# Kernel tuning notes

Hardware: AMD Instinct MI355X
Metric: run time of the kernel (lower is better)

Reference implementation:

```python
import jax, jax.numpy as jnp
import numpy as np

B, N = 8, 2048
DIN, DH, DE = 32, 64, 64
R = 3          # number_relations
L = 3          # num_layers -> 1 first + 1 block + 1 last
PRED_IN = DH * (L - 1) + DE  # concat: 64*2 + 64 = 192
EPS_BN = 1e-5
EPS_NORM = 1e-12


def setup_inputs() -> dict:
    key = jax.random.key(0)
    ks = jax.random.split(key, 12)
    x = jax.random.normal(ks[0], (B, N, DIN), jnp.float32)
    # relation labels in {0..R}; 0 = no edge, 1..R = relation type
    relation = jax.random.randint(ks[1], (B, N, N), 0, R + 1).astype(jnp.int32)
    # adjacency is the 0/1 edge indicator (float), as the torch code treats it
    adj = (relation > 0).astype(jnp.float32)
    s = 0.05
    w_first = jax.random.normal(ks[2], (R, DIN, DH), jnp.float32) * s
    b_first = jnp.zeros((DH,), jnp.float32)
    w_block = jax.random.normal(ks[3], (R, DH, DH), jnp.float32) * s
    b_block = jnp.zeros((DH,), jnp.float32)
    w_last = jax.random.normal(ks[4], (R, DH, DE), jnp.float32) * s
    b_last = jnp.zeros((DE,), jnp.float32)
    w_map = jax.random.normal(ks[5], (PRED_IN, DE), jnp.float32) * s
    b_map = jnp.zeros((DE,), jnp.float32)
    return {"x": x, "relation": relation, "adj": adj,
            "w_first": w_first, "b_first": b_first,
            "w_block": w_block, "b_block": b_block,
            "w_last": w_last, "b_last": b_last,
            "w_map": w_map, "b_map": b_map}


def _graph_conv(x, rel, W, b):
    # rel: [B,N,N] (int labels or float adjacency); W: [R, din, dout]
    y = jnp.zeros((x.shape[0], x.shape[1], W.shape[2]), x.dtype)
    for i in range(R):  # fixed, small relation count
        mask = (rel == (i + 1)).astype(x.dtype)            # [B,N,N]
        h = jnp.einsum('bij,bjd->bid', mask, x)            # masked aggregation
        y = y + jnp.einsum('bid,de->bie', h, W[i])
    y = y + b
    # F.normalize(p=2, dim=2): v / max(||v||, eps)
    nrm = jnp.sqrt(jnp.sum(y * y, axis=2, keepdims=True))
    return y / jnp.maximum(nrm, EPS_NORM)


def _apply_bn(x):
    # fresh BatchNorm1d(N) in training mode, affine weight=1/bias=0:
    # normalize over (batch, feature) per node index, biased variance
    mean = jnp.mean(x, axis=(0, 2), keepdims=True)
    var = jnp.mean(jnp.square(x - mean), axis=(0, 2), keepdims=True)
    return (x - mean) * jax.lax.rsqrt(var + EPS_BN)


def reference(x, relation, adj, w_first, b_first, w_block, b_block,
              w_last, b_last, w_map, b_map):
    # conv_first uses `relation`
    h = _apply_bn(jax.nn.relu(_graph_conv(x, relation, w_first, b_first)))
    out_all = [jnp.max(h, axis=1)]
    # conv_block and conv_last are (faithfully) called with `adj` as relation
    h = _apply_bn(jax.nn.relu(_graph_conv(h, adj, w_block, b_block)))
    out_all.append(jnp.max(h, axis=1))
    h = _graph_conv(h, adj, w_last, b_last)
    out_all.append(jnp.max(h, axis=1))
    output = jnp.concatenate(out_all, axis=1)        # [B, PRED_IN]
    ypred = output @ w_map + b_map                   # map_model Linear
    return (output, ypred)
```

## Files before the change

### kernel.cpp

```cpp
#include <hip/hip_runtime.h>


#define NN 2048
#define PLANE_W 1048576L

typedef short short8 __attribute__((ext_vector_type(8)));
typedef float floatx4 __attribute__((ext_vector_type(4)));

__device__ __forceinline__ unsigned short f2bf(float x) {
  unsigned u = __float_as_uint(x);
  u += 0x7FFFu + ((u >> 16) & 1u);
  return (unsigned short)(u >> 16);
}

__device__ void dev_xw_first(char* smemc, int u, int tid,
                             const float* __restrict__ x,
                             const float* __restrict__ w,
                             unsigned short* __restrict__ xws) {
  float* xs = (float*)smemc;
  float* wsh = (float*)(smemc + 64 * 33 * 4);
  const int jc = u & 31, b = (u >> 5) & 7, r = u >> 8;
  const int j0 = jc * 64;
  for (int idx = tid; idx < 64 * 32; idx += 256) {
    int row = idx >> 5, f = idx & 31;
    xs[row * 33 + f] = x[((long)b * NN + j0 + row) * 32 + f];
    wsh[idx] = w[r * 2048 + idx];
  }
  __syncthreads();
  const int j = tid & 63, g = tid >> 6;
  const int k = j0 + j;
  const int kblk = k >> 5, kq = (k >> 3) & 3, kj = k & 7;
  unsigned short* dst =
      xws + (((long)(r * 8 + b) * 64 + kblk) * 4 + g) * 512 + kj;
  float xr[32];
#pragma unroll
  for (int f = 0; f < 32; ++f) xr[f] = xs[j * 33 + f];
#pragma unroll
  for (int ii = 0; ii < 16; ++ii) {
    float acc = 0.f;
#pragma unroll
    for (int f = 0; f < 32; ++f) acc += xr[f] * wsh[f * 64 + g * 16 + ii];
    dst[(kq * 16 + ii) * 8] = f2bf(acc);
  }
  __syncthreads();
}

__global__ __launch_bounds__(256) void k_pack_xw1(const int* __restrict__ rel,
                                                  unsigned* __restrict__ planes,
                                                  const float* __restrict__ x,
                                                  const float* __restrict__ w,
                                                  unsigned short* __restrict__ xws) {
  __shared__ __align__(16) char smem[16640];
  const int bid = blockIdx.x, tid = threadIdx.x;
  if (bid < 768) dev_xw_first(smem, bid, tid, x, w, xws);
  for (long t = (long)bid * 256 + tid; t < 1048576L; t += 4096L * 256) {
    int w32 = (int)(t & 63);
    long bi = t >> 6;
    const int4* rp = (const int4*)(rel + bi * NN + w32 * 32);
    unsigned m0 = 0, m1 = 0, m2 = 0;
#pragma unroll
    for (int c = 0; c < 8; ++c) {
      int4 v = rp[c];
      int vv[4] = {v.x, v.y, v.z, v.w};
#pragma unroll
      for (int j = 0; j < 4; ++j) {
        unsigned b1 = 1u << (c * 4 + j);
        m0 |= (vv[j] == 1) ? b1 : 0u;
        m1 |= (vv[j] == 2) ? b1 : 0u;
        m2 |= (vv[j] == 3) ? b1 : 0u;
      }
    }
    long o = bi * 64 + w32;
    planes[o] = m0;
    planes[PLANE_W + o] = m1;
    planes[2 * PLANE_W + o] = m2;
  }
}

template <int NREL, bool RELU, bool POOL3>
__global__ __launch_bounds__(256) void k_gemm_f(
    const unsigned* __restrict__ planes, const unsigned short* __restrict__ xws,
    const float* __restrict__ bias, float* __restrict__ Hout,
    float* __restrict__ part3) {
  constexpr int SMEM = (NREL * 16640 > 32768) ? NREL * 16640 : 32768;
  __shared__ __align__(16) char smem[SMEM];
  unsigned* mw = (unsigned*)smem;
  floatx4* cb = (floatx4*)smem;
  const int bid = blockIdx.x;
  const int b = bid & 7, it = bid >> 3;
  const int tid = threadIdx.x;
  const int wave = tid >> 6, lane = tid & 63;
  const int m = lane & 15, kq = lane >> 4;
  const int i0 = it * 64;

  for (int idx = tid; idx < NREL * 4096; idx += 256) {
    int p = idx >> 12, rem = idx & 4095, row = rem >> 6, w = rem & 63;
    long g = ((long)b * NN + i0 + row) * 64 + w;
    unsigned v;
    if (NREL == 3)
      v = planes[(long)p * PLANE_W + g];
    else
      v = planes[g] | planes[PLANE_W + g] | planes[2 * PLANE_W + g];
    mw[(p * 64 + row) * 65 + w] = v;
  }
  __syncthreads();

  floatx4 acc[4][4];
#pragma unroll
  for (int rs = 0; rs < 4; ++rs)
#pragma unroll
    for (int t = 0; t < 4; ++t) acc[rs][t] = floatx4{0, 0, 0, 0};

  short8 bf[2][NREL][4];
  {
    const int kblk0 = wave * 16;
#pragma unroll
    for (int p = 0; p < NREL; ++p) {
      const unsigned short* bb =
          xws + ((long)(p * 8 + b) * 64 + kblk0) * 2048 + lane * 8;
#pragma unroll
      for (int t = 0; t < 4; ++t) bf[0][p][t] = *(const short8*)(bb + t * 512);
    }
  }
#pragma unroll 2
  for (int qq = 0; qq < 16; ++qq) {
    const int cur = qq & 1, nxt = cur ^ 1;
    if (qq < 15) {
      const int kblkn = wave * 16 + qq + 1;
#pragma unroll
      for (int p = 0; p < NREL; ++p) {
        const unsigned short* bb =
            xws + ((long)(p * 8 + b) * 64 + kblkn) * 2048 + lane * 8;
#pragma unroll
        for (int t = 0; t < 4; ++t)
          bf[nxt][p][t] = *(const short8*)(bb + t * 512);
      }
    }
    const int kblk = wave * 16 + qq;
#pragma unroll
    for (int p = 0; p < NREL; ++p) {
#pragma unroll
      for (int rs = 0; rs < 4; ++rs) {
        unsigned word = mw[(p * 64 + rs * 16 + m) * 65 + kblk];
        unsigned byte = (word >> (kq * 8)) & 0xffu;
        unsigned pp = byte | (byte << 15);
        union {
          unsigned uu[4];
          short8 s8;
        } fr;
        unsigned w0 = pp & 0x00010001u;
        fr.uu[0] = (w0 << 14) - (w0 << 7);
        unsigned w1 = pp & 0x00040004u;
        fr.uu[1] = (w1 << 12) - (w1 << 5);
        unsigned w2 = pp & 0x00100010u;
        fr.uu[2] = (w2 << 10) - (w2 << 3);
        unsigned w3 = pp & 0x00400040u;
        fr.uu[3] = (w3 << 8) - (w3 << 1);
#pragma unroll
        for (int t = 0; t < 4; ++t)
          acc[rs][t] = __builtin_amdgcn_mfma_f32_16x16x32_bf16(
              fr.s8, bf[cur][p][t], acc[rs][t], 0, 0, 0);
      }
    }
  }
  __syncthreads();

  if (wave >= 2) {
    floatx4* dst = cb + (wave - 2) * 1024;
#pragma unroll
    for (int rs = 0; rs < 4; ++rs)
#pragma unroll
      for (int t = 0; t < 4; ++t) dst[(rs * 4 + t) * 64 + lane] = acc[rs][t];
  }
  __syncthreads();
  if (wave < 2) {
    floatx4* src = cb + wave * 1024;
#pragma unroll
    for (int rs = 0; rs < 4; ++rs)
#pragma unroll
      for (int t = 0; t < 4; ++t) acc[rs][t] += src[(rs * 4 + t) * 64 + lane];
  }
  __syncthreads();
  if (wave == 1) {
#pragma unroll
    for (int rs = 0; rs < 4; ++rs)
#pragma unroll
      for (int t = 0; t < 4; ++t) cb[(rs * 4 + t) * 64 + lane] = acc[rs][t];
  }
  __syncthreads();
  if (wave == 0) {
#pragma unroll
    for (int rs = 0; rs < 4; ++rs)
#pragma unroll
      for (int t = 0; t < 4; ++t) acc[rs][t] += cb[(rs * 4 + t) * 64 + lane];
    float bv[4];
#pragma unroll
    for (int t = 0; t < 4; ++t) bv[t] = bias[t * 16 + m];
    float pmt[4] = {-3.4e38f, -3.4e38f, -3.4e38f, -3.4e38f};
#pragma unroll
    for (int rs = 0; rs < 4; ++rs) {
      float ss[4];
#pragma unroll
      for (int reg = 0; reg < 4; ++reg) {
#pragma unroll
        for (int t = 0; t < 4; ++t) acc[rs][t][reg] += bv[t];
        ss[reg] = acc[rs][0][reg] * acc[rs][0][reg] +
                  acc[rs][1][reg] * acc[rs][1][reg] +
                  acc[rs][2][reg] * acc[rs][2][reg] +
                  acc[rs][3][reg] * acc[rs][3][reg];
#pragma unroll
        for (int off = 1; off <= 8; off <<= 1)
          ss[reg] += __shfl_xor(ss[reg], off);
        ss[reg] = 1.0f / fmaxf(sqrtf(ss[reg]), 1e-12f);
      }
#pragma unroll
      for (int t = 0; t < 4; ++t) {
#pragma unroll
        for (int reg = 0; reg < 4; ++reg) {
          float o = acc[rs][t][reg] * ss[reg];
          if (RELU) o = fmaxf(o, 0.0f);
          if (POOL3)
            pmt[t] = fmaxf(pmt[t], o);
          else
            Hout[((long)b * NN + i0 + rs * 16 + kq * 4 + reg) * 64 + t * 16 + m] = o;
        }
      }
    }
    if (POOL3) {
#pragma unroll
      for (int t = 0; t < 4; ++t) {
        pmt[t] = fmaxf(pmt[t], __shfl_xor(pmt[t], 16));
        pmt[t] = fmaxf(pmt[t], __shfl_xor(pmt[t], 32));
      }
      if (kq == 0) {
#pragma unroll
        for (int t = 0; t < 4; ++t)
          part3[((long)b * 32 + it) * 64 + t * 16 + m] = pmt[t];
      }
    }
  }
}

__global__ __launch_bounds__(256) void k_bn(const float* __restrict__ Hs,
                                            float* __restrict__ HBNs,
                                            float* __restrict__ PP) {
  __shared__ float red[8];
  __shared__ float nv0[512];
  const int bid = blockIdx.x, tid = threadIdx.x;
  const int lane = tid & 63, wv = tid >> 6;
  const int wl = (wv & 1) * 64 + lane;
  const int flat0 = wl * 4;
  const int b = flat0 >> 6, e0 = flat0 & 63;
  const int np = bid;
  const int node = np * 2 + (wv >> 1);
  const float4 hv = *(const float4*)(Hs + ((long)b * NN + node) * 64 + e0);
  float s1 = hv.x + hv.y + hv.z + hv.w;
  float s2 = hv.x * hv.x + hv.y * hv.y + hv.z * hv.z + hv.w * hv.w;
#pragma unroll
  for (int off = 32; off >= 1; off >>= 1) {
    s1 += __shfl_xor(s1, off);
    s2 += __shfl_xor(s2, off);
  }
  if (lane == 0) {
    red[wv * 2] = s1;
    red[wv * 2 + 1] = s2;
  }
  __syncthreads();
  const int pb = (wv >> 1) * 4;
  float S1 = red[pb] + red[pb + 2];
  float S2 = red[pb + 1] + red[pb + 3];
  float mean = S1 * (1.0f / 512.0f);
  float var = fmaxf(S2 * (1.0f / 512.0f) - mean * mean, 0.0f);
  float rs = rsqrtf(var + 1e-5f);
  float4 nv;
  nv.x = (hv.x - mean) * rs;
  nv.y = (hv.y - mean) * rs;
  nv.z = (hv.z - mean) * rs;
  nv.w = (hv.w - mean) * rs;
  *(float4*)(HBNs + ((long)b * NN + node) * 64 + e0) = nv;
  if (wv < 2) *(float4*)(nv0 + flat0) = nv;
  __syncthreads();
  if (wv >= 2) {
    float4 ov = *(const float4*)(nv0 + flat0);
    float4 mx;
    mx.x = fmaxf(nv.x, ov.x);
    mx.y = fmaxf(nv.y, ov.y);
    mx.z = fmaxf(nv.z, ov.z);
    mx.w = fmaxf(nv.w, ov.w);
    *(float4*)(PP + (long)np * 512 + flat0) = mx;
  }
}

__global__ __launch_bounds__(256) void k_xwh_pf(const float* __restrict__ hsrc,
                                                const float* __restrict__ w,
                                                unsigned short* __restrict__ xws,
                                                const float* __restrict__ PP,
                                                float* __restrict__ out, int ofs) {
  __shared__ __align__(16) char smemc[33024];
  const int bid = blockIdx.x, tid = threadIdx.x;
  if (bid < 256) {
    float* hs = (float*)smemc;
    float* wsh = (float*)(smemc + 16640);
    const int jc = bid & 31, b = bid >> 5;
    const int j0 = jc * 64;
    for (int idx = tid; idx < 4096; idx += 256) {
      int row = idx >> 6, f = idx & 63;
      hs[row * 65 + f] = hsrc[((long)b * NN + j0 + row) * 64 + f];
      wsh[idx] = w[idx];
    }
    __syncthreads();
    const int j = tid & 63, g = tid >> 6;
    const int k = j0 + j;
    const int kblk = k >> 5, kq = (k >> 3) & 3, kj = k & 7;
    unsigned short* dst = xws + (((long)b * 64 + kblk) * 4 + g) * 512 + kj;
    float acc[16];
#pragma unroll
    for (int ii = 0; ii < 16; ++ii) acc[ii] = 0.f;
#pragma unroll
    for (int c = 0; c < 4; ++c) {
      float xr[16];
#pragma unroll
      for (int f = 0; f < 16; ++f) xr[f] = hs[j * 65 + c * 16 + f];
#pragma unroll
      for (int ii = 0; ii < 16; ++ii)
#pragma unroll
        for (int f = 0; f < 16; ++f)
          acc[ii] += xr[f] * wsh[(c * 16 + f) * 64 + g * 16 + ii];
    }
#pragma unroll
    for (int ii = 0; ii < 16; ++ii) dst[(kq * 16 + ii) * 8] = f2bf(acc[ii]);
  } else {
    const int b = bid - 256;
    const int e = tid & 63, q = tid >> 6;
    float m = -3.4e38f;
    for (int blk = q; blk < 1024; blk += 4)
      m = fmaxf(m, PP[(long)blk * 512 + b * 64 + e]);
    float* pmx = (float*)smemc;
    pmx[q * 64 + e] = m;
    __syncthreads();
    if (q == 0)
      out[b * 192 + ofs + e] =
          fmaxf(fmaxf(pmx[e], pmx[64 + e]), fmaxf(pmx[128 + e], pmx[192 + e]));
  }
}

__global__ __launch_bounds__(512) void k_tail(const float* __restrict__ P3,
                                              float* __restrict__ out,
                                              const float* __restrict__ wmap,
                                              const float* __restrict__ bmap) {
  const int b = threadIdx.x >> 6, e = threadIdx.x & 63;
  float m = -3.4e38f;
#pragma unroll
  for (int c = 0; c < 32; ++c) m = fmaxf(m, P3[((long)b * 32 + c) * 64 + e]);
  out[b * 192 + 128 + e] = m;
  __syncthreads();
  float acc = bmap[e];
  for (int k = 0; k < 192; ++k) acc += out[b * 192 + k] * wmap[k * 64 + e];
  out[1536 + b * 64 + e] = acc;
}

extern "C" void kernel_launch(void* const* d_in, const int* in_sizes, int n_in,
                              void* d_out, int out_size, void* d_ws,
                              size_t ws_size, hipStream_t stream) {
  const float* x = (const float*)d_in[0];
  const int* rel = (const int*)d_in[1];
  const float* w_first = (const float*)d_in[3];
  const float* b_first = (const float*)d_in[4];
  const float* w_block = (const float*)d_in[5];
  const float* b_block = (const float*)d_in[6];
  const float* w_last = (const float*)d_in[7];
  const float* b_last = (const float*)d_in[8];
  const float* w_map = (const float*)d_in[9];
  const float* b_map = (const float*)d_in[10];
  float* out = (float*)d_out;

  char* ws = (char*)d_ws;
  const size_t MB = 1024 * 1024;
  unsigned* PLANES = (unsigned*)(ws);
  unsigned short* XWS = (unsigned short*)(ws + 12 * MB);
  float* H = (float*)(ws + 18 * MB);
  float* HBN = (float*)(ws + 22 * MB);
  float* PARTP = (float*)(ws + 26 * MB);
  float* PART3 = (float*)(ws + 28 * MB);

  k_pack_xw1<<<4096, 256, 0, stream>>>(rel, PLANES, x, w_first, XWS);
  k_gemm_f<3, true, false><<<256, 256, 0, stream>>>(PLANES, XWS, b_first, H,
                                                    nullptr);
  k_bn<<<1024, 256, 0, stream>>>(H, HBN, PARTP);
  k_xwh_pf<<<264, 256, 0, stream>>>(HBN, w_block, XWS, PARTP, out, 0);
  k_gemm_f<1, true, false><<<256, 256, 0, stream>>>(PLANES, XWS, b_block, H,
                                                    nullptr);
  k_bn<<<1024, 256, 0, stream>>>(H, HBN, PARTP);
  k_xwh_pf<<<264, 256, 0, stream>>>(HBN, w_last, XWS, PARTP, out, 64);
  k_gemm_f<1, false, true><<<256, 256, 0, stream>>>(PLANES, XWS, b_last,
                                                    nullptr, PART3);
  k_tail<<<1, 512, 0, stream>>>(PART3, out, w_map, b_map);
}
```

Measured before the change: 427.8 us.

## Fuse batchnorm into XW transform and widen aggregation GEMM to eight waves

The separate batchnorm kernel is folded into the XW-transform kernel: each block recomputes the per-node mean and variance over all batches, normalizes in shared memory, and writes per-node-chunk max partials. The pooled max reductions for layers one and two move into the tail kernel. The masked-aggregation GEMM now runs 512 threads (8 waves) with the bitmask tile loaded in two K chunks and a serial cross-wave reduction. This removes two launches and the HBN round trip through memory, at the cost of redundant statistics reads across batch blocks and more synchronisation in the reduction.

```diff
diff --git a/kernel.cpp b/kernel.cpp
--- a/kernel.cpp
+++ b/kernel.cpp
@@ -78,11 +78,11 @@
 }
 
 template <int NREL, bool RELU, bool POOL3>
-__global__ __launch_bounds__(256) void k_gemm_f(
+__global__ __launch_bounds__(512) void k_gemm8(
     const unsigned* __restrict__ planes, const unsigned short* __restrict__ xws,
     const float* __restrict__ bias, float* __restrict__ Hout,
     float* __restrict__ part3) {
-  constexpr int SMEM = (NREL * 16640 > 32768) ? NREL * 16640 : 32768;
+  constexpr int SMEM = (NREL * 8448 > 16640) ? NREL * 8448 : 16640;
   __shared__ __align__(16) char smem[SMEM];
   unsigned* mw = (unsigned*)smem;
   floatx4* cb = (floatx4*)smem;
@@ -93,101 +93,86 @@
   const int m = lane & 15, kq = lane >> 4;
   const int i0 = it * 64;
 
-  for (int idx = tid; idx < NREL * 4096; idx += 256) {
-    int p = idx >> 12, rem = idx & 4095, row = rem >> 6, w = rem & 63;
-    long g = ((long)b * NN + i0 + row) * 64 + w;
-    unsigned v;
-    if (NREL == 3)
-      v = planes[(long)p * PLANE_W + g];
-    else
-      v = planes[g] | planes[PLANE_W + g] | planes[2 * PLANE_W + g];
-    mw[(p * 64 + row) * 65 + w] = v;
-  }
-  __syncthreads();
-
   floatx4 acc[4][4];
 #pragma unroll
   for (int rs = 0; rs < 4; ++rs)
 #pragma unroll
     for (int t = 0; t < 4; ++t) acc[rs][t] = floatx4{0, 0, 0, 0};
 
-  short8 bf[2][NREL][4];
-  {
-    const int kblk0 = wave * 16;
-#pragma unroll
-    for (int p = 0; p < NREL; ++p) {
-      const unsigned short* bb =
-          xws + ((long)(p * 8 + b) * 64 + kblk0) * 2048 + lane * 8;
-#pragma unroll
-      for (int t = 0; t < 4; ++t) bf[0][p][t] = *(const short8*)(bb + t * 512);
-    }
-  }
-#pragma unroll 2
-  for (int qq = 0; qq < 16; ++qq) {
-    const int cur = qq & 1, nxt = cur ^ 1;
-    if (qq < 15) {
-      const int kblkn = wave * 16 + qq + 1;
+  for (int chunk = 0; chunk < 2; ++chunk) {
+    for (int idx = tid; idx < NREL * 2048; idx += 512) {
+      int p = idx >> 11, rem = idx & 2047, row = rem >> 5, w = rem & 31;
+      long g = ((long)b * NN + i0 + row) * 64 + chunk * 32 + w;
+      unsigned v;
+      if (NREL == 3)
+        v = planes[(long)p * PLANE_W + g];
+      else
+        v = planes[g] | planes[PLANE_W + g] | planes[2 * PLANE_W + g];
+      mw[(p * 64 + row) * 33 + w] = v;
+    }
+    __syncthreads();
+#pragma unroll
+    for (int j = 0; j < 4; ++j) {
+      const int kk = j * 8 + wave;
+      const int kblk = chunk * 32 + kk;
 #pragma unroll
       for (int p = 0; p < NREL; ++p) {
         const unsigned short* bb =
-            xws + ((long)(p * 8 + b) * 64 + kblkn) * 2048 + lane * 8;
-#pragma unroll
-        for (int t = 0; t < 4; ++t)
-          bf[nxt][p][t] = *(const short8*)(bb + t * 512);
-      }
-    }
-    const int kblk = wave * 16 + qq;
-#pragma unroll
-    for (int p = 0; p < NREL; ++p) {
-#pragma unroll
-      for (int rs = 0; rs < 4; ++rs) {
-        unsigned word = mw[(p * 64 + rs * 16 + m) * 65 + kblk];
-        unsigned byte = (word >> (kq * 8)) & 0xffu;
-        unsigned pp = byte | (byte << 15);
-        union {
-          unsigned uu[4];
-          short8 s8;
-        } fr;
-        unsigned w0 = pp & 0x00010001u;
-        fr.uu[0] = (w0 << 14) - (w0 << 7);
-        unsigned w1 = pp & 0x00040004u;
-        fr.uu[1] = (w1 << 12) - (w1 << 5);
-        unsigned w2 = pp & 0x00100010u;
-        fr.uu[2] = (w2 << 10) - (w2 << 3);
-        unsigned w3 = pp & 0x00400040u;
-        fr.uu[3] = (w3 << 8) - (w3 << 1);
-#pragma unroll
-        for (int t = 0; t < 4; ++t)
-          acc[rs][t] = __builtin_amdgcn_mfma_f32_16x16x32_bf16(
-              fr.s8, bf[cur][p][t], acc[rs][t], 0, 0, 0);
-      }
-    }
-  }
-  __syncthreads();
-
-  if (wave >= 2) {
-    floatx4* dst = cb + (wave - 2) * 1024;
-#pragma unroll
-    for (int rs = 0; rs < 4; ++rs)
-#pragma unroll
-      for (int t = 0; t < 4; ++t) dst[(rs * 4 + t) * 64 + lane] = acc[rs][t];
-  }
-  __syncthreads();
-  if (wave < 2) {
-    floatx4* src = cb + wave * 1024;
-#pragma unroll
-    for (int rs = 0; rs < 4; ++rs)
-#pragma unroll
-      for (int t = 0; t < 4; ++t) acc[rs][t] += src[(rs * 4 + t) * 64 + lane];
-  }
-  __syncthreads();
-  if (wave == 1) {
-#pragma unroll
-    for (int rs = 0; rs < 4; ++rs)
-#pragma unroll
-      for (int t = 0; t < 4; ++t) cb[(rs * 4 + t) * 64 + lane] = acc[rs][t];
-  }
-  __syncthreads();
+            xws + ((long)(p * 8 + b) * 64 + kblk) * 2048 + lane * 8;
+        short8 bf0 = *(const short8*)(bb);
+        short8 bf1 = *(const short8*)(bb + 512);
+        short8 bf2 = *(const short8*)(bb + 1024);
+        short8 bf3 = *(const short8*)(bb + 1536);
+#pragma unroll
+        for (int rs = 0; rs < 4; ++rs) {
+          unsigned word = mw[(p * 64 + rs * 16 + m) * 33 + kk];
+          unsigned byte = (word >> (kq * 8)) & 0xffu;
+          unsigned pp = byte | (byte << 15);
+          union {
+            unsigned uu[4];
+            short8 s8;
+          } fr;
+          unsigned w0 = pp & 0x00010001u;
+          fr.uu[0] = (w0 << 14) - (w0 << 7);
+          unsigned w1 = pp & 0x00040004u;
+          fr.uu[1] = (w1 << 12) - (w1 << 5);
+          unsigned w2 = pp & 0x00100010u;
+          fr.uu[2] = (w2 << 10) - (w2 << 3);
+          unsigned w3 = pp & 0x00400040u;
+          fr.uu[3] = (w3 << 8) - (w3 << 1);
+          acc[rs][0] = __builtin_amdgcn_mfma_f32_16x16x32_bf16(fr.s8, bf0,
+                                                              acc[rs][0], 0, 0, 0);
+          acc[rs][1] = __builtin_amdgcn_mfma_f32_16x16x32_bf16(fr.s8, bf1,
+                                                              acc[rs][1], 0, 0, 0);
+          acc[rs][2] = __builtin_amdgcn_mfma_f32_16x16x32_bf16(fr.s8, bf2,
+                                                              acc[rs][2], 0, 0, 0);
+          acc[rs][3] = __builtin_amdgcn_mfma_f32_16x16x32_bf16(fr.s8, bf3,
+                                                              acc[rs][3], 0, 0, 0);
+        }
+      }
+    }
+    __syncthreads();
+  }
+
+  for (int k = 7; k >= 1; --k) {
+    if (wave == k) {
+      if (k == 7) {
+#pragma unroll
+        for (int rs = 0; rs < 4; ++rs)
+#pragma unroll
+          for (int t = 0; t < 4; ++t) cb[(rs * 4 + t) * 64 + lane] = acc[rs][t];
+      } else {
+#pragma unroll
+        for (int rs = 0; rs < 4; ++rs)
+#pragma unroll
+          for (int t = 0; t < 4; ++t) {
+            floatx4 v = cb[(rs * 4 + t) * 64 + lane];
+            cb[(rs * 4 + t) * 64 + lane] = v + acc[rs][t];
+          }
+      }
+    }
+    __syncthreads();
+  }
   if (wave == 0) {
 #pragma unroll
     for (int rs = 0; rs < 4; ++rs)
@@ -241,74 +226,50 @@
   }
 }
 
-__global__ __launch_bounds__(256) void k_bn(const float* __restrict__ Hs,
-                                            float* __restrict__ HBNs,
-                                            float* __restrict__ PP) {
-  __shared__ float red[8];
-  __shared__ float nv0[512];
-  const int bid = blockIdx.x, tid = threadIdx.x;
-  const int lane = tid & 63, wv = tid >> 6;
-  const int wl = (wv & 1) * 64 + lane;
-  const int flat0 = wl * 4;
-  const int b = flat0 >> 6, e0 = flat0 & 63;
-  const int np = bid;
-  const int node = np * 2 + (wv >> 1);
-  const float4 hv = *(const float4*)(Hs + ((long)b * NN + node) * 64 + e0);
-  float s1 = hv.x + hv.y + hv.z + hv.w;
-  float s2 = hv.x * hv.x + hv.y * hv.y + hv.z * hv.z + hv.w * hv.w;
-#pragma unroll
-  for (int off = 32; off >= 1; off >>= 1) {
-    s1 += __shfl_xor(s1, off);
-    s2 += __shfl_xor(s2, off);
-  }
-  if (lane == 0) {
-    red[wv * 2] = s1;
-    red[wv * 2 + 1] = s2;
-  }
-  __syncthreads();
-  const int pb = (wv >> 1) * 4;
-  float S1 = red[pb] + red[pb + 2];
-  float S2 = red[pb + 1] + red[pb + 3];
-  float mean = S1 * (1.0f / 512.0f);
-  float var = fmaxf(S2 * (1.0f / 512.0f) - mean * mean, 0.0f);
-  float rs = rsqrtf(var + 1e-5f);
-  float4 nv;
-  nv.x = (hv.x - mean) * rs;
-  nv.y = (hv.y - mean) * rs;
-  nv.z = (hv.z - mean) * rs;
-  nv.w = (hv.w - mean) * rs;
-  *(float4*)(HBNs + ((long)b * NN + node) * 64 + e0) = nv;
-  if (wv < 2) *(float4*)(nv0 + flat0) = nv;
-  __syncthreads();
-  if (wv >= 2) {
-    float4 ov = *(const float4*)(nv0 + flat0);
-    float4 mx;
-    mx.x = fmaxf(nv.x, ov.x);
-    mx.y = fmaxf(nv.y, ov.y);
-    mx.z = fmaxf(nv.z, ov.z);
-    mx.w = fmaxf(nv.w, ov.w);
-    *(float4*)(PP + (long)np * 512 + flat0) = mx;
-  }
-}
-
-__global__ __launch_bounds__(256) void k_xwh_pf(const float* __restrict__ hsrc,
+__global__ __launch_bounds__(256) void k_xwh_bn(const float* __restrict__ H,
                                                 const float* __restrict__ w,
                                                 unsigned short* __restrict__ xws,
-                                                const float* __restrict__ PP,
-                                                float* __restrict__ out, int ofs) {
-  __shared__ __align__(16) char smemc[33024];
+                                                float* __restrict__ PP) {
+  __shared__ float hs[64 * 65];
+  __shared__ float wsh[64 * 64];
+  __shared__ float sm[64], srs[64];
   const int bid = blockIdx.x, tid = threadIdx.x;
-  if (bid < 256) {
-    float* hs = (float*)smemc;
-    float* wsh = (float*)(smemc + 16640);
-    const int jc = bid & 31, b = bid >> 5;
-    const int j0 = jc * 64;
-    for (int idx = tid; idx < 4096; idx += 256) {
-      int row = idx >> 6, f = idx & 63;
-      hs[row * 65 + f] = hsrc[((long)b * NN + j0 + row) * 64 + f];
-      wsh[idx] = w[idx];
-    }
-    __syncthreads();
+  const int jc = bid & 31, b = bid >> 5;
+  const int j0 = jc * 64;
+  {
+    const int n = tid >> 2, q = tid & 3;
+    float s1 = 0.f, s2 = 0.f;
+#pragma unroll
+    for (int bb = 0; bb < 8; ++bb) {
+      const float4* hp =
+          (const float4*)(H + ((long)bb * NN + j0 + n) * 64 + q * 16);
+#pragma unroll
+      for (int c = 0; c < 4; ++c) {
+        float4 v = hp[c];
+        s1 += v.x + v.y + v.z + v.w;
+        s2 += v.x * v.x + v.y * v.y + v.z * v.z + v.w * v.w;
+      }
+    }
+    s1 += __shfl_xor(s1, 1);
+    s2 += __shfl_xor(s2, 1);
+    s1 += __shfl_xor(s1, 2);
+    s2 += __shfl_xor(s2, 2);
+    if (q == 0) {
+      float mean = s1 * (1.0f / 512.0f);
+      float var = fmaxf(s2 * (1.0f / 512.0f) - mean * mean, 0.0f);
+      sm[n] = mean;
+      srs[n] = rsqrtf(var + 1e-5f);
+    }
+  }
+  __syncthreads();
+  for (int idx = tid; idx < 4096; idx += 256) {
+    int row = idx >> 6, f = idx & 63;
+    float v = H[((long)b * NN + j0 + row) * 64 + f];
+    hs[row * 65 + f] = (v - sm[row]) * srs[row];
+    wsh[idx] = w[idx];
+  }
+  __syncthreads();
+  {
     const int j = tid & 63, g = tid >> 6;
     const int k = j0 + j;
     const int kblk = k >> 5, kq = (k >> 3) & 3, kj = k & 7;
@@ -329,34 +290,44 @@
     }
 #pragma unroll
     for (int ii = 0; ii < 16; ++ii) dst[(kq * 16 + ii) * 8] = f2bf(acc[ii]);
-  } else {
-    const int b = bid - 256;
-    const int e = tid & 63, q = tid >> 6;
-    float m = -3.4e38f;
-    for (int blk = q; blk < 1024; blk += 4)
-      m = fmaxf(m, PP[(long)blk * 512 + b * 64 + e]);
-    float* pmx = (float*)smemc;
-    pmx[q * 64 + e] = m;
-    __syncthreads();
-    if (q == 0)
-      out[b * 192 + ofs + e] =
-          fmaxf(fmaxf(pmx[e], pmx[64 + e]), fmaxf(pmx[128 + e], pmx[192 + e]));
-  }
-}
-
-__global__ __launch_bounds__(512) void k_tail(const float* __restrict__ P3,
+  }
+  if (b == 0) {
+#pragma unroll
+    for (int part = 0; part < 2; ++part) {
+      const int col = part * 256 + tid;
+      const int bb = col >> 6, e = col & 63;
+      float mx = -3.4e38f;
+      for (int n = 0; n < 64; ++n) {
+        float v = H[((long)bb * NN + j0 + n) * 64 + e];
+        mx = fmaxf(mx, (v - sm[n]) * srs[n]);
+      }
+      PP[(long)jc * 512 + col] = mx;
+    }
+  }
+}
+
+__global__ __launch_bounds__(512) void k_tail(const float* __restrict__ PP1,
+                                              const float* __restrict__ PP2,
+                                              const float* __restrict__ P3,
                                               float* __restrict__ out,
                                               const float* __restrict__ wmap,
                                               const float* __restrict__ bmap) {
-  const int b = threadIdx.x >> 6, e = threadIdx.x & 63;
-  float m = -3.4e38f;
-#pragma unroll
-  for (int c = 0; c < 32; ++c) m = fmaxf(m, P3[((long)b * 32 + c) * 64 + e]);
-  out[b * 192 + 128 + e] = m;
+  const int col = threadIdx.x;
+  const int bb = col >> 6, e = col & 63;
+  float m1 = -3.4e38f, m2 = -3.4e38f, m3 = -3.4e38f;
+#pragma unroll
+  for (int c = 0; c < 32; ++c) {
+    m1 = fmaxf(m1, PP1[(long)c * 512 + col]);
+    m2 = fmaxf(m2, PP2[(long)c * 512 + col]);
+    m3 = fmaxf(m3, P3[((long)bb * 32 + c) * 64 + e]);
+  }
+  out[bb * 192 + e] = m1;
+  out[bb * 192 + 64 + e] = m2;
+  out[bb * 192 + 128 + e] = m3;
   __syncthreads();
   float acc = bmap[e];
-  for (int k = 0; k < 192; ++k) acc += out[b * 192 + k] * wmap[k * 64 + e];
-  out[1536 + b * 64 + e] = acc;
+  for (int k = 0; k < 192; ++k) acc += out[bb * 192 + k] * wmap[k * 64 + e];
+  out[1536 + bb * 64 + e] = acc;
 }
 
 extern "C" void kernel_launch(void* const* d_in, const int* in_sizes, int n_in,
@@ -379,20 +350,18 @@
   unsigned* PLANES = (unsigned*)(ws);
   unsigned short* XWS = (unsigned short*)(ws + 12 * MB);
   float* H = (float*)(ws + 18 * MB);
-  float* HBN = (float*)(ws + 22 * MB);
-  float* PARTP = (float*)(ws + 26 * MB);
-  float* PART3 = (float*)(ws + 28 * MB);
+  float* PP1 = (float*)(ws + 22 * MB);
+  float* PP2 = (float*)(ws + 23 * MB);
+  float* PART3 = (float*)(ws + 24 * MB);
 
   k_pack_xw1<<<4096, 256, 0, stream>>>(rel, PLANES, x, w_first, XWS);
-  k_gemm_f<3, true, false><<<256, 256, 0, stream>>>(PLANES, XWS, b_first, H,
-                                                    nullptr);
-  k_bn<<<1024, 256, 0, stream>>>(H, HBN, PARTP);
-  k_xwh_pf<<<264, 256, 0, stream>>>(HBN, w_block, XWS, PARTP, out, 0);
-  k_gemm_f<1, true, false><<<256, 256, 0, stream>>>(PLANES, XWS, b_block, H,
-                                                    nullptr);
-  k_bn<<<1024, 256, 0, stream>>>(H, HBN, PARTP);
-  k_xwh_pf<<<264, 256, 0, stream>>>(HBN, w_last, XWS, PARTP, out, 64);
-  k_gemm_f<1, false, true><<<256, 256, 0, stream>>>(PLANES, XWS, b_last,
-                                                    nullptr, PART3);
-  k_tail<<<1, 512, 0, stream>>>(PART3, out, w_map, b_map);
-}
+  k_gemm8<3, true, false><<<256, 512, 0, stream>>>(PLANES, XWS, b_first, H,
+                                                   nullptr);
+  k_xwh_bn<<<256, 256, 0, stream>>>(H, w_block, XWS, PP1);
+  k_gemm8<1, true, false><<<256, 512, 0, stream>>>(PLANES, XWS, b_block, H,
+                                                   nullptr);
+  k_xwh_bn<<<256, 256, 0, stream>>>(H, w_last, XWS, PP2);
+  k_gemm8<1, false, true><<<256, 512, 0, stream>>>(PLANES, XWS, b_last,
+                                                   nullptr, PART3);
+  k_tail<<<1, 512, 0, stream>>>(PP1, PP2, PART3, out, w_map, b_map);
+}
```

After: 353.3 us. 1.21x faster.
